# Kernel optimization log

Measured on AMD Instinct MI355X. Metric: run time of the kernel, lower is better.

Reference implementation:

```python
import jax, jax.numpy as jnp
import numpy as np

N_USERS = 50000
N_ITEMS = 40000
D = 64
E = 1_000_000
NB = 3       # behaviors
L = 2        # GCN layers per behavior
B = 8192
N_NODES = (N_USERS + 1) + (N_ITEMS + 1)
REG_WEIGHT = 0.01
CL_TEMP = 0.1
BPR_GAMMA = 1e-10


def setup_inputs() -> dict:
    key = jax.random.key(0)
    k1, k2, k3, k4, k5 = jax.random.split(key, 5)
    user_emb = jax.random.normal(k1, (N_USERS + 1, D), jnp.float32) * 0.1
    item_emb = jax.random.normal(k2, (N_ITEMS + 1, D), jnp.float32) * 0.1
    gcn_w = jax.random.normal(k3, (NB, L, D, D), jnp.float32) * 0.1
    gcn_b = jnp.zeros((NB, L, D), jnp.float32)
    edge_index = jax.random.randint(k4, (NB, 2, E), 0, N_NODES, dtype=jnp.int64)
    batch_data = jax.random.randint(k5, (B, NB, 3), 0, 40000, dtype=jnp.int64)
    return {"user_emb": user_emb, "item_emb": item_emb, "gcn_w": gcn_w,
            "gcn_b": gcn_b, "edge_index": edge_index, "batch_data": batch_data}


def gcn_layer(x, edge_index, W, b):
    # PyG GCNConv(add_self_loops=False): h = x @ W; out[col] += norm * h[row]; out += b
    row, col = edge_index[0], edge_index[1]
    n = x.shape[0]
    deg = jnp.zeros((n,), x.dtype).at[col].add(1.0)
    dinv = jnp.where(deg > 0, jax.lax.rsqrt(jnp.maximum(deg, 1.0)), 0.0)
    norm = dinv[row] * dinv[col]                    # [E]
    h = x @ W                                       # [N, D]
    msg = h[row] * norm[:, None]                    # [E, D] gather
    out = jnp.zeros_like(x).at[col].add(msg)        # scatter-add
    return out + b


def _cos(a, b):
    num = jnp.sum(a * b, axis=-1)
    den = jnp.maximum(jnp.linalg.norm(a, axis=-1) * jnp.linalg.norm(b, axis=-1), 1e-8)
    return num / den


def reference(user_emb, item_emb, gcn_w, gcn_b, edge_index, batch_data):
    total = jnp.concatenate([user_emb, item_emb], axis=0)   # [N_NODES, D]
    total_loss = jnp.float32(0.0)
    te = total
    for bi in range(NB):
        # gcn propagate for this behavior (eval: dropout is identity)
        le = te
        for l in range(L):
            le = gcn_layer(le, edge_index[bi], gcn_w[bi, l], gcn_b[bi, l])
        # F.normalize(dim=-1)
        le = le / jnp.maximum(jnp.linalg.norm(le, axis=-1, keepdims=True), 1e-12)
        te = le + te
        # losses for this behavior
        users = batch_data[:, bi, 0]
        items = batch_data[:, bi, 1:]                        # [B, 2]
        ue = te[:N_USERS + 1]
        ie = te[N_USERS + 1:]
        uf = ue[users]                                       # [B, D]
        itf = ie[items]                                      # [B, 2, D]
        pos, neg = itf[:, 0], itf[:, 1]
        # info-nce (cross-entropy over [pos, neg] cosine sims, label 0)
        logits = jnp.stack([_cos(uf, pos), _cos(uf, neg)], axis=1) / CL_TEMP
        cl_loss = jnp.mean(-jax.nn.log_softmax(logits, axis=-1)[:, 0])
        # BPR loss (weight per behavior = 1.0)
        scores = jnp.sum(uf[:, None, :] * itf, axis=2)       # [B, 2]
        bpr = jnp.mean(-jnp.log(BPR_GAMMA + jax.nn.sigmoid(scores[:, 0] - scores[:, 1])))
        total_loss = total_loss + bpr + cl_loss
    # EmbLoss: sum of L2 norms of the raw embedding tables / last table's rows
    emb_loss = (jnp.linalg.norm(user_emb) + jnp.linalg.norm(item_emb)) / item_emb.shape[0]
    return total_loss + REG_WEIGHT * emb_loss
```

## Files before the change

kernel.cpp:

```cpp
#include <hip/hip_runtime.h>
#include <hip/hip_fp16.h>
#include <math.h>

#define NU 50001
#define NI 40001
#define NNODES 90002
#define DD 64
#define EE 1000000
#define NBB 3
#define LL 2
#define BB 8192
#define STRIDE 40
#define QS 16.0f
#define T4U (NU * 16)
#define T4T (NNODES * 16)
#define NBIN 352
#define NPAD (NBIN * 256)
#define CHUNK 4096
#define NBLK 245
#define SCANL (NBIN * NBLK)
#define SCB 337

__global__ __launch_bounds__(256) void k_hist(const int* __restrict__ edge, unsigned* __restrict__ Hb) {
    __shared__ unsigned h[NBIN];
    int bi = blockIdx.y, blk = blockIdx.x, tid = threadIdx.x;
    for (int i = tid; i < NBIN; i += 256) h[i] = 0;
    __syncthreads();
    const int* colp = edge + (size_t)bi * 2 * EE + EE;
    int base = blk * CHUNK;
    #pragma unroll
    for (int k = 0; k < CHUNK / 256; k++) {
        int e = base + k * 256 + tid;
        if (e < EE) atomicAdd(&h[(unsigned)colp[e] >> 8], 1u);
    }
    __syncthreads();
    for (int i = tid; i < NBIN; i += 256)
        Hb[(size_t)bi * SCANL + (size_t)i * NBLK + blk] = h[i];
}

__global__ __launch_bounds__(256) void k_scan1(unsigned* __restrict__ Hb, unsigned* __restrict__ bsum) {
    __shared__ unsigned s[256];
    int bi = blockIdx.y;
    int i = blockIdx.x * 256 + threadIdx.x;
    unsigned v = (i < SCANL) ? Hb[(size_t)bi * SCANL + i] : 0u;
    s[threadIdx.x] = v;
    __syncthreads();
    #pragma unroll
    for (int o = 1; o < 256; o <<= 1) {
        unsigned t = (threadIdx.x >= o) ? s[threadIdx.x - o] : 0u;
        __syncthreads();
        s[threadIdx.x] += t;
        __syncthreads();
    }
    if (i < SCANL) Hb[(size_t)bi * SCANL + i] = s[threadIdx.x] - v;
    if (threadIdx.x == 255) bsum[bi * SCB + blockIdx.x] = s[255];
}

__global__ __launch_bounds__(512) void k_scan2(unsigned* __restrict__ bsum) {
    __shared__ unsigned s[512];
    int bi = blockIdx.y;
    int t = threadIdx.x;
    unsigned v = (t < SCB) ? bsum[bi * SCB + t] : 0u;
    s[t] = v;
    __syncthreads();
    #pragma unroll
    for (int o = 1; o < 512; o <<= 1) {
        unsigned u = (t >= o) ? s[t - o] : 0u;
        __syncthreads();
        s[t] += u;
        __syncthreads();
    }
    if (t < SCB) bsum[bi * SCB + t] = s[t] - v;
}

__global__ __launch_bounds__(256) void k_scan3(unsigned* __restrict__ Hb, const unsigned* __restrict__ bsum) {
    int bi = blockIdx.y;
    int i = blockIdx.x * 256 + threadIdx.x;
    if (i < SCANL) Hb[(size_t)bi * SCANL + i] += bsum[bi * SCB + blockIdx.x];
}

__global__ __launch_bounds__(256) void k_scatp(const int* __restrict__ edge, const unsigned* __restrict__ Hb,
                                               uint2* __restrict__ binbuf) {
    __shared__ unsigned posc[NBIN];
    int bi = blockIdx.y, blk = blockIdx.x, tid = threadIdx.x;
    for (int i = tid; i < NBIN; i += 256)
        posc[i] = Hb[(size_t)bi * SCANL + (size_t)i * NBLK + blk];
    __syncthreads();
    const int* rowp = edge + (size_t)bi * 2 * EE;
    const int* colp = rowp + EE;
    uint2* bb = binbuf + (size_t)bi * EE;
    int base = blk * CHUNK;
    #pragma unroll
    for (int k = 0; k < CHUNK / 256; k++) {
        int e = base + k * 256 + tid;
        if (e < EE) {
            unsigned c = (unsigned)colp[e];
            unsigned pos = atomicAdd(&posc[c >> 8], 1u);
            uint2 pr; pr.x = c; pr.y = (unsigned)rowp[e];
            bb[pos] = pr;
        }
    }
}

__global__ __launch_bounds__(256) void k_bucket(const unsigned* __restrict__ Hb, const uint2* __restrict__ binbuf,
                                                unsigned* __restrict__ cnt3, unsigned* __restrict__ bucket3) {
    __shared__ unsigned lb[256 * STRIDE];
    __shared__ unsigned cl[256];
    int bi = blockIdx.y, bin = blockIdx.x, tid = threadIdx.x;
    cl[tid] = 0;
    __syncthreads();
    unsigned s0 = Hb[(size_t)bi * SCANL + (size_t)bin * NBLK];
    unsigned s1 = (bin + 1 < NBIN) ? Hb[(size_t)bi * SCANL + (size_t)(bin + 1) * NBLK] : (unsigned)EE;
    const uint2* bb = binbuf + (size_t)bi * EE;
    for (unsigned i = s0 + tid; i < s1; i += 256) {
        uint2 pr = bb[i];
        unsigned c = pr.x - ((unsigned)bin << 8);
        unsigned pos = atomicAdd(&cl[c], 1u);
        if (pos < STRIDE) lb[c * STRIDE + pos] = pr.y;
    }
    __syncthreads();
    cnt3[(size_t)bi * NPAD + (size_t)bin * 256 + tid] = cl[tid];
    uint4* dst = (uint4*)(bucket3 + (size_t)bi * NPAD * STRIDE + (size_t)bin * 256 * STRIDE);
    const uint4* srcl = (const uint4*)lb;
    #pragma unroll
    for (int k = 0; k < (256 * STRIDE / 4) / 256; k++)
        dst[k * 256 + tid] = srcl[k * 256 + tid];
}

__global__ __launch_bounds__(256) void k_init(const float* __restrict__ user_emb,
                                              const float* __restrict__ item_emb,
                                              const unsigned* __restrict__ cnt0,
                                              float* __restrict__ te, unsigned* __restrict__ X8a,
                                              float* __restrict__ scal) {
    int i0 = blockIdx.x * 256 + threadIdx.x;
    int stride = gridDim.x * 256;
    float su = 0.f, si = 0.f;
    const float4* u4 = (const float4*)user_emb;
    const float4* i4 = (const float4*)item_emb;
    float4* t4 = (float4*)te;
    for (int i = i0; i < T4T; i += stride) {
        float4 v;
        if (i < T4U) { v = u4[i]; su += v.x * v.x + v.y * v.y + v.z * v.z + v.w * v.w; }
        else         { v = i4[i - T4U]; si += v.x * v.x + v.y * v.y + v.z * v.z + v.w * v.w; }
        t4[i] = v;
        unsigned d = cnt0[i >> 4];
        float q = (d ? rsqrtf((float)d) : 0.f) * QS;
        int p0 = __builtin_amdgcn_cvt_pk_fp8_f32(v.x * q, v.y * q, 0, false);
        p0 = __builtin_amdgcn_cvt_pk_fp8_f32(v.z * q, v.w * q, p0, true);
        X8a[i] = (unsigned)p0;
    }
    #pragma unroll
    for (int o = 32; o > 0; o >>= 1) { su += __shfl_down(su, o); si += __shfl_down(si, o); }
    __shared__ float lsu[4], lsi[4];
    int w = threadIdx.x >> 6;
    if ((threadIdx.x & 63) == 0) { lsu[w] = su; lsi[w] = si; }
    __syncthreads();
    if (threadIdx.x == 0) {
        atomicAdd(scal + 1, lsu[0] + lsu[1] + lsu[2] + lsu[3]);
        atomicAdd(scal + 2, lsi[0] + lsi[1] + lsi[2] + lsi[3]);
    }
}

__global__ __launch_bounds__(256) void k_agg(const unsigned* __restrict__ cnt,
                                             const unsigned* __restrict__ bucket,
                                             const uint2* __restrict__ X8in,
                                             __half* __restrict__ agg) {
    int t = blockIdx.x * 256 + threadIdx.x;
    int r = t >> 6;
    if (r >= NNODES) return;
    int lane = t & 63;
    int j2 = lane & 7;
    int hw = lane >> 3;
    unsigned d = cnt[r];
    unsigned dc = d < STRIDE ? d : STRIDE;
    const unsigned* bk = bucket + (size_t)r * STRIDE;
    unsigned a0 = (hw +  0 < dc) ? bk[hw +  0] : (unsigned)NNODES;
    unsigned a1 = (hw +  8 < dc) ? bk[hw +  8] : (unsigned)NNODES;
    unsigned a2 = (hw + 16 < dc) ? bk[hw + 16] : (unsigned)NNODES;
    unsigned a3 = (hw + 24 < dc) ? bk[hw + 24] : (unsigned)NNODES;
    uint2 w0 = X8in[(size_t)a0 * 8 + j2];
    uint2 w1 = X8in[(size_t)a1 * 8 + j2];
    uint2 w2 = X8in[(size_t)a2 * 8 + j2];
    uint2 w3 = X8in[(size_t)a3 * 8 + j2];
    float4 A = {0.f, 0.f, 0.f, 0.f}, Bv = {0.f, 0.f, 0.f, 0.f};
#define ACC8(W) { \
    A.x  += __builtin_amdgcn_cvt_f32_fp8((int)W.x, 0); \
    A.y  += __builtin_amdgcn_cvt_f32_fp8((int)W.x, 1); \
    A.z  += __builtin_amdgcn_cvt_f32_fp8((int)W.x, 2); \
    A.w  += __builtin_amdgcn_cvt_f32_fp8((int)W.x, 3); \
    Bv.x += __builtin_amdgcn_cvt_f32_fp8((int)W.y, 0); \
    Bv.y += __builtin_amdgcn_cvt_f32_fp8((int)W.y, 1); \
    Bv.z += __builtin_amdgcn_cvt_f32_fp8((int)W.y, 2); \
    Bv.w += __builtin_amdgcn_cvt_f32_fp8((int)W.y, 3); }
    ACC8(w0) ACC8(w1) ACC8(w2) ACC8(w3)
    for (unsigned i = hw + 32; i < dc; i += 8) {
        uint2 w = X8in[(size_t)bk[i] * 8 + j2];
        ACC8(w)
    }
#undef ACC8
    #pragma unroll
    for (int o = 8; o <= 32; o <<= 1) {
        A.x  += __shfl_xor(A.x, o);  A.y  += __shfl_xor(A.y, o);
        A.z  += __shfl_xor(A.z, o);  A.w  += __shfl_xor(A.w, o);
        Bv.x += __shfl_xor(Bv.x, o); Bv.y += __shfl_xor(Bv.y, o);
        Bv.z += __shfl_xor(Bv.z, o); Bv.w += __shfl_xor(Bv.w, o);
    }
    if (hw == 0) {
        union { __half2 h[4]; float4 f; } u;
        u.h[0] = __floats2half2_rn(A.x, A.y);
        u.h[1] = __floats2half2_rn(A.z, A.w);
        u.h[2] = __floats2half2_rn(Bv.x, Bv.y);
        u.h[3] = __floats2half2_rn(Bv.z, Bv.w);
        ((float4*)agg)[(size_t)r * 8 + j2] = u.f;
    }
}

template <int FUSE>
__global__ __launch_bounds__(256) void k_gemmE(const __half* __restrict__ agg, const float* __restrict__ W,
                                               const float* __restrict__ b, const unsigned* __restrict__ cnt,
                                               float* __restrict__ te, unsigned* __restrict__ X8out,
                                               const unsigned* __restrict__ cnt_next) {
    __shared__ float ws[64 * 64];
    __shared__ float xs[16][64];
    int tid = threadIdx.x;
    #pragma unroll
    for (int q = 0; q < 4; q++)
        ((float4*)ws)[tid + q * 256] = ((const float4*)W)[tid + q * 256];
    int r0 = blockIdx.x * 16;
    {
        int rr = r0 + (tid >> 4);
        int cc = (tid & 15) * 4;
        if (rr < NNODES) {
            uint2 u = ((const uint2*)agg)[(size_t)rr * 16 + (tid & 15)];
            union { unsigned u; __half2 h; } c0, c1;
            c0.u = u.x; c1.u = u.y;
            float2 f0 = __half22float2(c0.h);
            float2 f1 = __half22float2(c1.h);
            xs[tid >> 4][cc + 0] = f0.x; xs[tid >> 4][cc + 1] = f0.y;
            xs[tid >> 4][cc + 2] = f1.x; xs[tid >> 4][cc + 3] = f1.y;
        }
    }
    __syncthreads();
    int rloc = tid >> 4;
    int j = tid & 15;
    int d4 = j * 4;
    int row = r0 + rloc;
    if (row >= NNODES) return;
    float4 acc = {0.f, 0.f, 0.f, 0.f};
    #pragma unroll
    for (int k = 0; k < 64; k++) {
        float xv = xs[rloc][k];
        float4 wv = *(const float4*)&ws[k * 64 + d4];
        acc.x += xv * wv.x; acc.y += xv * wv.y;
        acc.z += xv * wv.z; acc.w += xv * wv.w;
    }
    unsigned d = cnt[row];
    float m = (d ? rsqrtf((float)d) : 0.f) * (1.0f / QS);
    float4 bb = ((const float4*)b)[j];
    float vx = acc.x * m + bb.x;
    float vy = acc.y * m + bb.y;
    float vz = acc.z * m + bb.z;
    float vw = acc.w * m + bb.w;
    if (FUSE == 0) {
        unsigned dn = cnt_next[row];
        float q = (dn ? rsqrtf((float)dn) : 0.f) * QS;
        int p0 = __builtin_amdgcn_cvt_pk_fp8_f32(vx * q, vy * q, 0, false);
        p0 = __builtin_amdgcn_cvt_pk_fp8_f32(vz * q, vw * q, p0, true);
        X8out[(size_t)row * 16 + j] = (unsigned)p0;
    } else {
        float s = vx * vx + vy * vy + vz * vz + vw * vw;
        #pragma unroll
        for (int o = 1; o <= 8; o <<= 1) s += __shfl_xor(s, o);
        float scale = 1.f / fmaxf(sqrtf(s), 1e-12f);
        float4* te4 = (float4*)te;
        float4 old = te4[(size_t)row * 16 + j];
        old.x += vx * scale; old.y += vy * scale;
        old.z += vz * scale; old.w += vw * scale;
        te4[(size_t)row * 16 + j] = old;
        if (X8out) {
            unsigned dn = cnt_next[row];
            float q = (dn ? rsqrtf((float)dn) : 0.f) * QS;
            int p0 = __builtin_amdgcn_cvt_pk_fp8_f32(old.x * q, old.y * q, 0, false);
            p0 = __builtin_amdgcn_cvt_pk_fp8_f32(old.z * q, old.w * q, p0, true);
            X8out[(size_t)row * 16 + j] = (unsigned)p0;
        }
    }
}

__global__ __launch_bounds__(256) void k_loss(const float* __restrict__ te, const int* __restrict__ batch,
                                              int bi, float* __restrict__ acc) {
    int t = blockIdx.x * 256 + threadIdx.x;
    int s = t >> 6;
    int lane = t & 63;
    if (s >= BB) return;
    const int* bd = &batch[s * (NBB * 3) + bi * 3];
    int u = bd[0], p = bd[1], n = bd[2];
    float uv = te[(size_t)u * DD + lane];
    float pv = te[(size_t)(NU + p) * DD + lane];
    float nv = te[(size_t)(NU + n) * DD + lane];
    float d_up = uv * pv, d_un = uv * nv;
    float s_u = uv * uv, s_p = pv * pv, s_n = nv * nv;
    for (int o = 32; o > 0; o >>= 1) {
        d_up += __shfl_xor(d_up, o);
        d_un += __shfl_xor(d_un, o);
        s_u  += __shfl_xor(s_u, o);
        s_p  += __shfl_xor(s_p, o);
        s_n  += __shfl_xor(s_n, o);
    }
    __shared__ float part[4];
    if (lane == 0) {
        float cosp = d_up / fmaxf(sqrtf(s_u) * sqrtf(s_p), 1e-8f);
        float cosn = d_un / fmaxf(sqrtf(s_u) * sqrtf(s_n), 1e-8f);
        float cl = log1pf(expf((cosn - cosp) * 10.0f));
        float sig = 1.f / (1.f + expf(-(d_up - d_un)));
        float bpr = -logf(1e-10f + sig);
        part[(threadIdx.x >> 6) & 3] = cl + bpr;
    }
    __syncthreads();
    if (threadIdx.x == 0)
        atomicAdd(acc, (part[0] + part[1] + part[2] + part[3]) * (1.0f / BB));
}

__global__ void k_final(const float* __restrict__ scal, float* __restrict__ out) {
    if (threadIdx.x == 0 && blockIdx.x == 0)
        out[0] = scal[0] + 0.01f * (sqrtf(scal[1]) + sqrtf(scal[2])) / 40001.0f;
}

extern "C" void kernel_launch(void* const* d_in, const int* in_sizes, int n_in,
                              void* d_out, int out_size, void* d_ws, size_t ws_size,
                              hipStream_t stream) {
    const float* user_emb = (const float*)d_in[0];
    const float* item_emb = (const float*)d_in[1];
    const float* gcn_w    = (const float*)d_in[2];
    const float* gcn_b    = (const float*)d_in[3];
    const int*   edge_idx = (const int*)d_in[4];
    const int*   batch    = (const int*)d_in[5];
    float* out = (float*)d_out;

    char* ws = (char*)d_ws;
    size_t off = 0;
    auto alloc = [&](size_t bytes) {
        void* p = ws + off;
        off = (off + bytes + 255) & ~(size_t)255;
        return p;
    };
    float*    te      = (float*)alloc((size_t)NNODES * DD * sizeof(float));
    __half*   agg     = (__half*)alloc((size_t)NNODES * DD * sizeof(__half));
    unsigned* X8a     = (unsigned*)alloc((size_t)(NNODES + 1) * 16 * sizeof(unsigned));
    unsigned* X8b     = (unsigned*)alloc((size_t)(NNODES + 1) * 16 * sizeof(unsigned));
    unsigned* cnt3    = (unsigned*)alloc((size_t)NBB * NPAD * sizeof(unsigned));
    unsigned* bucket3 = (unsigned*)alloc((size_t)NBB * NPAD * STRIDE * sizeof(unsigned));
    uint2*    binbuf  = (uint2*)alloc((size_t)NBB * EE * sizeof(uint2));
    unsigned* Hb      = (unsigned*)alloc((size_t)NBB * SCANL * sizeof(unsigned));
    unsigned* bsum    = (unsigned*)alloc((size_t)NBB * SCB * sizeof(unsigned));
    float*    scal    = (float*)alloc(64 * sizeof(float));

    hipMemsetAsync(scal, 0, 64 * sizeof(float), stream);
    hipMemsetAsync(X8a + (size_t)NNODES * 16, 0, 64, stream);
    hipMemsetAsync(X8b + (size_t)NNODES * 16, 0, 64, stream);

    k_hist <<<dim3(NBLK, NBB), 256, 0, stream>>>(edge_idx, Hb);
    k_scan1<<<dim3(SCB,  NBB), 256, 0, stream>>>(Hb, bsum);
    k_scan2<<<dim3(1,    NBB), 512, 0, stream>>>(bsum);
    k_scan3<<<dim3(SCB,  NBB), 256, 0, stream>>>(Hb, bsum);
    k_scatp<<<dim3(NBLK, NBB), 256, 0, stream>>>(edge_idx, Hb, binbuf);
    k_bucket<<<dim3(NBIN, NBB), 256, 0, stream>>>(Hb, binbuf, cnt3, bucket3);

    k_init<<<1024, 256, 0, stream>>>(user_emb, item_emb, cnt3, te, X8a, scal);

    const int gat_grid  = (NNODES * DD + 255) / 256;
    const int gemm_grid = (NNODES + 15) / 16;

    for (int bi = 0; bi < NBB; bi++) {
        const unsigned* cnt = cnt3 + (size_t)bi * NPAD;
        const unsigned* bucket = bucket3 + (size_t)bi * NPAD * STRIDE;
        const float* W0 = gcn_w + ((size_t)bi * LL + 0) * DD * DD;
        const float* b0 = gcn_b + ((size_t)bi * LL + 0) * DD;
        const float* W1 = gcn_w + ((size_t)bi * LL + 1) * DD * DD;
        const float* b1 = gcn_b + ((size_t)bi * LL + 1) * DD;

        k_agg<<<gat_grid, 256, 0, stream>>>(cnt, bucket, (const uint2*)X8a, agg);
        k_gemmE<0><<<gemm_grid, 256, 0, stream>>>(agg, W0, b0, cnt, nullptr, X8b, cnt);

        k_agg<<<gat_grid, 256, 0, stream>>>(cnt, bucket, (const uint2*)X8b, agg);
        unsigned* x8next = (bi < NBB - 1) ? X8a : nullptr;
        const unsigned* cnt_next = cnt3 + (size_t)((bi + 1) % NBB) * NPAD;
        k_gemmE<1><<<gemm_grid, 256, 0, stream>>>(agg, W1, b1, cnt, te, x8next, cnt_next);

        k_loss<<<(BB * 64) / 256, 256, 0, stream>>>(te, batch, bi, scal);
    }

    k_final<<<1, 64, 0, stream>>>(scal, out);
}
```

Measured before the change: 505.2 us.

## Pack bin entries into one word and merge scan passes into a single kernel

Bin-sort preprocessing now packs the low column byte and the row index into one 32-bit word, which halves the intermediate binbuf traffic. The three-kernel prefix scan becomes one 1024-thread block per behavior that scans serially per thread, removing two launches and the bsum buffer. Chunk size and block size are doubled, so the histogram has fewer columns to scan. The packing assumes row indices fit in 17 bits (NNODES 90002 < 131072), and a single-block scan limits parallelism but only covers about 43K entries.

```diff
diff --git a/kernel.cpp b/kernel.cpp
--- a/kernel.cpp
+++ b/kernel.cpp
@@ -16,93 +16,79 @@
 #define T4T (NNODES * 16)
 #define NBIN 352
 #define NPAD (NBIN * 256)
-#define CHUNK 4096
-#define NBLK 245
+#define CHUNK 8192
+#define NBLK 123
 #define SCANL (NBIN * NBLK)
-#define SCB 337
-
-__global__ __launch_bounds__(256) void k_hist(const int* __restrict__ edge, unsigned* __restrict__ Hb) {
+#define SCTH 43
+
+__global__ __launch_bounds__(512) void k_hist(const int* __restrict__ edge, unsigned* __restrict__ Hb) {
     __shared__ unsigned h[NBIN];
     int bi = blockIdx.y, blk = blockIdx.x, tid = threadIdx.x;
-    for (int i = tid; i < NBIN; i += 256) h[i] = 0;
+    for (int i = tid; i < NBIN; i += 512) h[i] = 0;
     __syncthreads();
     const int* colp = edge + (size_t)bi * 2 * EE + EE;
     int base = blk * CHUNK;
-    #pragma unroll
-    for (int k = 0; k < CHUNK / 256; k++) {
-        int e = base + k * 256 + tid;
+    for (int k = 0; k < CHUNK / 512; k++) {
+        int e = base + k * 512 + tid;
         if (e < EE) atomicAdd(&h[(unsigned)colp[e] >> 8], 1u);
     }
     __syncthreads();
-    for (int i = tid; i < NBIN; i += 256)
+    for (int i = tid; i < NBIN; i += 512)
         Hb[(size_t)bi * SCANL + (size_t)i * NBLK + blk] = h[i];
 }
 
-__global__ __launch_bounds__(256) void k_scan1(unsigned* __restrict__ Hb, unsigned* __restrict__ bsum) {
-    __shared__ unsigned s[256];
+__global__ __launch_bounds__(1024) void k_scanall(unsigned* __restrict__ Hb) {
+    __shared__ unsigned ls[1024];
     int bi = blockIdx.y;
-    int i = blockIdx.x * 256 + threadIdx.x;
-    unsigned v = (i < SCANL) ? Hb[(size_t)bi * SCANL + i] : 0u;
-    s[threadIdx.x] = v;
-    __syncthreads();
-    #pragma unroll
-    for (int o = 1; o < 256; o <<= 1) {
-        unsigned t = (threadIdx.x >= o) ? s[threadIdx.x - o] : 0u;
+    unsigned* H = Hb + (size_t)bi * SCANL;
+    int t = threadIdx.x;
+    unsigned vals[SCTH];
+    unsigned s = 0;
+    int base = t * SCTH;
+    #pragma unroll
+    for (int k = 0; k < SCTH; k++) {
+        int idx = base + k;
+        unsigned v = (idx < SCANL) ? H[idx] : 0u;
+        vals[k] = v; s += v;
+    }
+    ls[t] = s;
+    __syncthreads();
+    for (int o = 1; o < 1024; o <<= 1) {
+        unsigned u = (t >= o) ? ls[t - o] : 0u;
         __syncthreads();
-        s[threadIdx.x] += t;
+        ls[t] += u;
         __syncthreads();
     }
-    if (i < SCANL) Hb[(size_t)bi * SCANL + i] = s[threadIdx.x] - v;
-    if (threadIdx.x == 255) bsum[bi * SCB + blockIdx.x] = s[255];
-}
-
-__global__ __launch_bounds__(512) void k_scan2(unsigned* __restrict__ bsum) {
-    __shared__ unsigned s[512];
-    int bi = blockIdx.y;
-    int t = threadIdx.x;
-    unsigned v = (t < SCB) ? bsum[bi * SCB + t] : 0u;
-    s[t] = v;
-    __syncthreads();
-    #pragma unroll
-    for (int o = 1; o < 512; o <<= 1) {
-        unsigned u = (t >= o) ? s[t - o] : 0u;
-        __syncthreads();
-        s[t] += u;
-        __syncthreads();
-    }
-    if (t < SCB) bsum[bi * SCB + t] = s[t] - v;
-}
-
-__global__ __launch_bounds__(256) void k_scan3(unsigned* __restrict__ Hb, const unsigned* __restrict__ bsum) {
-    int bi = blockIdx.y;
-    int i = blockIdx.x * 256 + threadIdx.x;
-    if (i < SCANL) Hb[(size_t)bi * SCANL + i] += bsum[bi * SCB + blockIdx.x];
-}
-
-__global__ __launch_bounds__(256) void k_scatp(const int* __restrict__ edge, const unsigned* __restrict__ Hb,
-                                               uint2* __restrict__ binbuf) {
+    unsigned run = ls[t] - s;
+    #pragma unroll
+    for (int k = 0; k < SCTH; k++) {
+        int idx = base + k;
+        if (idx < SCANL) { unsigned tmp = vals[k]; H[idx] = run; run += tmp; }
+    }
+}
+
+__global__ __launch_bounds__(512) void k_scatp(const int* __restrict__ edge, const unsigned* __restrict__ Hb,
+                                               unsigned* __restrict__ binbuf) {
     __shared__ unsigned posc[NBIN];
     int bi = blockIdx.y, blk = blockIdx.x, tid = threadIdx.x;
-    for (int i = tid; i < NBIN; i += 256)
+    for (int i = tid; i < NBIN; i += 512)
         posc[i] = Hb[(size_t)bi * SCANL + (size_t)i * NBLK + blk];
     __syncthreads();
     const int* rowp = edge + (size_t)bi * 2 * EE;
     const int* colp = rowp + EE;
-    uint2* bb = binbuf + (size_t)bi * EE;
+    unsigned* bb = binbuf + (size_t)bi * EE;
     int base = blk * CHUNK;
-    #pragma unroll
-    for (int k = 0; k < CHUNK / 256; k++) {
-        int e = base + k * 256 + tid;
+    for (int k = 0; k < CHUNK / 512; k++) {
+        int e = base + k * 512 + tid;
         if (e < EE) {
             unsigned c = (unsigned)colp[e];
             unsigned pos = atomicAdd(&posc[c >> 8], 1u);
-            uint2 pr; pr.x = c; pr.y = (unsigned)rowp[e];
-            bb[pos] = pr;
+            bb[pos] = ((c & 255u) << 17) | (unsigned)rowp[e];
         }
     }
 }
 
-__global__ __launch_bounds__(256) void k_bucket(const unsigned* __restrict__ Hb, const uint2* __restrict__ binbuf,
+__global__ __launch_bounds__(256) void k_bucket(const unsigned* __restrict__ Hb, const unsigned* __restrict__ binbuf,
                                                 unsigned* __restrict__ cnt3, unsigned* __restrict__ bucket3) {
     __shared__ unsigned lb[256 * STRIDE];
     __shared__ unsigned cl[256];
@@ -111,12 +97,12 @@
     __syncthreads();
     unsigned s0 = Hb[(size_t)bi * SCANL + (size_t)bin * NBLK];
     unsigned s1 = (bin + 1 < NBIN) ? Hb[(size_t)bi * SCANL + (size_t)(bin + 1) * NBLK] : (unsigned)EE;
-    const uint2* bb = binbuf + (size_t)bi * EE;
+    const unsigned* bb = binbuf + (size_t)bi * EE;
     for (unsigned i = s0 + tid; i < s1; i += 256) {
-        uint2 pr = bb[i];
-        unsigned c = pr.x - ((unsigned)bin << 8);
+        unsigned pr = bb[i];
+        unsigned c = pr >> 17;
         unsigned pos = atomicAdd(&cl[c], 1u);
-        if (pos < STRIDE) lb[c * STRIDE + pos] = pr.y;
+        if (pos < STRIDE) lb[c * STRIDE + pos] = pr & 0x1FFFFu;
     }
     __syncthreads();
     cnt3[(size_t)bi * NPAD + (size_t)bin * 256 + tid] = cl[tid];
@@ -350,21 +336,18 @@
     unsigned* X8b     = (unsigned*)alloc((size_t)(NNODES + 1) * 16 * sizeof(unsigned));
     unsigned* cnt3    = (unsigned*)alloc((size_t)NBB * NPAD * sizeof(unsigned));
     unsigned* bucket3 = (unsigned*)alloc((size_t)NBB * NPAD * STRIDE * sizeof(unsigned));
-    uint2*    binbuf  = (uint2*)alloc((size_t)NBB * EE * sizeof(uint2));
+    unsigned* binbuf  = (unsigned*)alloc((size_t)NBB * EE * sizeof(unsigned));
     unsigned* Hb      = (unsigned*)alloc((size_t)NBB * SCANL * sizeof(unsigned));
-    unsigned* bsum    = (unsigned*)alloc((size_t)NBB * SCB * sizeof(unsigned));
     float*    scal    = (float*)alloc(64 * sizeof(float));
 
     hipMemsetAsync(scal, 0, 64 * sizeof(float), stream);
     hipMemsetAsync(X8a + (size_t)NNODES * 16, 0, 64, stream);
     hipMemsetAsync(X8b + (size_t)NNODES * 16, 0, 64, stream);
 
-    k_hist <<<dim3(NBLK, NBB), 256, 0, stream>>>(edge_idx, Hb);
-    k_scan1<<<dim3(SCB,  NBB), 256, 0, stream>>>(Hb, bsum);
-    k_scan2<<<dim3(1,    NBB), 512, 0, stream>>>(bsum);
-    k_scan3<<<dim3(SCB,  NBB), 256, 0, stream>>>(Hb, bsum);
-    k_scatp<<<dim3(NBLK, NBB), 256, 0, stream>>>(edge_idx, Hb, binbuf);
-    k_bucket<<<dim3(NBIN, NBB), 256, 0, stream>>>(Hb, binbuf, cnt3, bucket3);
+    k_hist   <<<dim3(NBLK, NBB), 512,  0, stream>>>(edge_idx, Hb);
+    k_scanall<<<dim3(1,    NBB), 1024, 0, stream>>>(Hb);
+    k_scatp  <<<dim3(NBLK, NBB), 512,  0, stream>>>(edge_idx, Hb, binbuf);
+    k_bucket <<<dim3(NBIN, NBB), 256,  0, stream>>>(Hb, binbuf, cnt3, bucket3);
 
     k_init<<<1024, 256, 0, stream>>>(user_emb, item_emb, cnt3, te, X8a, scal);
 
```

After: 536.6 us. +6.2%, slower.
